# Performance work log

Measured on AMD Instinct MI355X. Metric: run time of the kernel, lower is better.

Reference implementation:

```python
import jax, jax.numpy as jnp
import numpy as np

CLS_W = 1.0
REG_W = 1.0
POS_THR = 0.6
THR_LOW = 0.3
THR_HIGH = 0.6
N_POS = 16
N_NEG = 48
BATCH = 4096
NUM_ANCHOR = 5
FS = 17
SEARCH = 255


def make_anchors():
    # SiamRPN-style anchors: 5 aspect ratios, base size 64, stride 8, 17x17 grid
    ratios = np.array([0.33, 0.5, 1.0, 2.0, 3.0], dtype=np.float64)
    size, stride = 64.0, 8
    ws = np.sqrt(size * size / ratios)            # (K,)
    hs = ws * ratios                              # (K,)
    c = (np.arange(FS) - FS // 2) * stride + SEARCH // 2  # grid centers
    cx = np.broadcast_to(c[None, None, :], (NUM_ANCHOR, FS, FS))
    cy = np.broadcast_to(c[None, :, None], (NUM_ANCHOR, FS, FS))
    w = np.broadcast_to(ws[:, None, None], (NUM_ANCHOR, FS, FS))
    h = np.broadcast_to(hs[:, None, None], (NUM_ANCHOR, FS, FS))
    center = np.stack([cx, cy, w, h], 0).reshape(4, -1).T               # (A,4) cx,cy,w,h
    corner = np.stack([cx - w / 2, cy - h / 2, cx + w / 2, cy + h / 2], 0).reshape(4, -1).T
    return center.astype(np.float32), corner.astype(np.float32)


def setup_inputs() -> dict:
    key = jax.random.key(0)
    k1, k2, k3, k4 = jax.random.split(key, 4)
    pred_cls = jax.random.normal(k1, (BATCH, NUM_ANCHOR, FS, FS), dtype=jnp.float32)
    pred_reg = jax.random.normal(k2, (BATCH, 4, NUM_ANCHOR, FS, FS), dtype=jnp.float32)
    # valid GT boxes inside the search region, overlapping anchor sizes
    cxy = jax.random.uniform(k3, (BATCH, 2), minval=90.0, maxval=165.0)
    wh = jax.random.uniform(k4, (BATCH, 2), minval=35.0, maxval=110.0)
    gt_bbox = jnp.concatenate([cxy - wh / 2, cxy + wh / 2], axis=1).astype(jnp.float32)
    center, corner = make_anchors()
    return {
        "pred_cls": pred_cls,
        "pred_reg": pred_reg,
        "gt_bbox": gt_bbox,
        "anchor_center": jnp.asarray(center),
        "anchor_corner": jnp.asarray(corner),
    }


def jaccard(box_a, box_b):
    # box_a (N,4), box_b (A,4) in x1,y1,x2,y2 -> (N,A) IoU
    lt = jnp.maximum(box_a[:, None, :2], box_b[None, :, :2])
    rb = jnp.minimum(box_a[:, None, 2:], box_b[None, :, 2:])
    wh = jnp.clip(rb - lt, 0.0)
    inter = wh[..., 0] * wh[..., 1]
    area_a = (box_a[:, 2] - box_a[:, 0]) * (box_a[:, 3] - box_a[:, 1])
    area_b = (box_b[:, 2] - box_b[:, 0]) * (box_b[:, 3] - box_b[:, 1])
    return inter / (area_a[:, None] + area_b[None, :] - inter)


def _rand_rank(k, m, A):
    # rank of each index among masked entries under a random shuffle
    u = jax.random.uniform(k, (A,))
    s = jnp.where(m, u, jnp.inf)
    order = jnp.argsort(s)
    return jnp.zeros((A,), jnp.int32).at[order].set(jnp.arange(A, dtype=jnp.int32))


def _forward(pred_cls, pred_reg, gt_bbox, anchor_center, anchor_corner):
    N = pred_cls.shape[0]
    A = anchor_center.shape[0]
    iou = jaccard(gt_bbox, anchor_corner)                       # (N,A)
    matched = jnp.where(iou > THR_HIGH, 1.0, jnp.where(iou < THR_LOW, 0.0, -1.0))
    ks = jax.random.split(jax.random.key(42), 2 * N)
    kpos, kneg = ks[:N], ks[N:]

    def per_sample(cls, reg, gt, mask, kp, kn):
        clsf = cls.reshape(-1)                                  # (A,)
        regf = reg.reshape(4, -1).T                             # (A,4)
        pos = mask == 1.0
        neg = mask == 0.0
        n_pos = jnp.sum(pos).astype(jnp.int32)
        n_neg = jnp.sum(neg).astype(jnp.int32)
        rp = _rand_rank(kp, pos, A)
        rn = _rand_rank(kn, neg, A)
        k_p = jnp.minimum(n_pos, N_POS)                         # sampled positives
        k_n_cap = jnp.where(n_pos > 0, 3 * n_pos, N_NEG)        # int(n_pos*48/16) = 3*n_pos
        k_n = jnp.minimum(n_neg, k_n_cap)
        sel_p = pos & (rp < k_p)
        sel_n = neg & (rn < k_n)
        bce_p = jnp.logaddexp(0.0, -clsf)                       # BCEWithLogits, target 1
        bce_n = jnp.logaddexp(0.0, clsf)                        # BCEWithLogits, target 0
        denom = jnp.maximum(k_p + k_n, 1).astype(clsf.dtype)
        loss_cls_i = (jnp.sum(bce_p * sel_p) + jnp.sum(bce_n * sel_n)) / denom
        acc_i = (jnp.sum((clsf >= POS_THR) & pos) + jnp.sum((clsf < POS_THR) & (~pos))).astype(clsf.dtype) / A
        gcx = (gt[0] + gt[2]) * 0.5
        gcy = (gt[1] + gt[3]) * 0.5
        gw = gt[2] - gt[0]
        gh = gt[3] - gt[1]
        acx, acy, aw, ah = anchor_center[:, 0], anchor_center[:, 1], anchor_center[:, 2], anchor_center[:, 3]
        tgt = jnp.stack([(gcx - acx) / aw, (gcy - acy) / ah, jnp.log(gw / aw), jnp.log(gh / ah)], axis=1)
        np_safe = jnp.maximum(n_pos, 1).astype(clsf.dtype)
        loss_reg_i = jnp.where(n_pos > 0,
                               jnp.sum(((regf - tgt) ** 2) * pos[:, None]) / (4.0 * np_safe),
                               0.0)
        return loss_cls_i, loss_reg_i, acc_i

    lc, lr, ac = jax.vmap(per_sample)(pred_cls, pred_reg, gt_bbox, matched, kpos, kneg)
    loss_cls = jnp.mean(lc)
    loss_reg = jnp.mean(lr)
    acc_cls = jnp.mean(ac)
    loss_total = CLS_W * loss_cls + REG_W * loss_reg
    return loss_total, loss_cls, loss_reg, acc_cls


def reference(pred_cls, pred_reg, gt_bbox, anchor_center, anchor_corner):
    return _forward(pred_cls, pred_reg, gt_bbox, anchor_center, anchor_corner)
```

## Files before the change

kernel.cpp:

```cpp
#include <hip/hip_runtime.h>
#include <stdint.h>
#include <math.h>


#define A_TOT 1445
#define NITER 23
#define WPB 4
#define POS_MAX 64
#define CAND_MAX 128

__device__ __forceinline__ void tf2x32(uint32_t k0, uint32_t k1, uint32_t x0, uint32_t x1,
                                       uint32_t& o0, uint32_t& o1)
{
  const uint32_t k2 = k0 ^ k1 ^ 0x1BD11BDAu;
  x0 += k0; x1 += k1;
#define TFR(r) { x0 += x1; x1 = __builtin_rotateleft32(x1, (r)); x1 ^= x0; }
  TFR(13) TFR(15) TFR(26) TFR(6)
  x0 += k1; x1 += k2 + 1u;
  TFR(17) TFR(29) TFR(16) TFR(24)
  x0 += k2; x1 += k0 + 2u;
  TFR(13) TFR(15) TFR(26) TFR(6)
  x0 += k0; x1 += k1 + 3u;
  TFR(17) TFR(29) TFR(16) TFR(24)
  x0 += k1; x1 += k2 + 4u;
  TFR(13) TFR(15) TFR(26) TFR(6)
  x0 += k2; x1 += k0 + 5u;
#undef TFR
  o0 = x0; o1 = x1;
}

__device__ __forceinline__ float lae0(float x){
  return fmaxf(x, 0.0f) + __logf(1.0f + __expf(-fabsf(x)));
}

__global__ void __launch_bounds__(WPB * 64, 4) rpn_loss_kernel(
    const float* __restrict__ pred_cls, const float* __restrict__ pred_reg,
    const float* __restrict__ gt_bbox, const float* __restrict__ anchor_center,
    const float* __restrict__ anchor_corner,
    float* __restrict__ part,
    int N)
{
  __shared__ uint32_t s_hist[WPB][256];
  __shared__ uint32_t s_cand[WPB][CAND_MAX];
  __shared__ uint32_t s_pidx[WPB][POS_MAX];
  __shared__ float    s_pcls[WPB][POS_MAX];
  __shared__ uint32_t s_cnt[WPB][2];

  const int w    = threadIdx.x >> 6;
  const int lane = threadIdx.x & 63;
  const int n    = blockIdx.x * WPB + w;

  #pragma unroll
  for (int b = 0; b < 4; b++) s_hist[w][lane * 4 + b] = 0u;
  if (lane < 2) s_cnt[w][lane] = 0u;

  const float g0 = gt_bbox[4 * n + 0];
  const float g1 = gt_bbox[4 * n + 1];
  const float g2 = gt_bbox[4 * n + 2];
  const float g3 = gt_bbox[4 * n + 3];
  const float area_a = (g2 - g0) * (g3 - g1);

  uint32_t kp0, kp1, kn0, kn1;
  tf2x32(0u, 42u, 0u, (uint32_t)n,       kp0, kp1);
  tf2x32(0u, 42u, 0u, (uint32_t)(N + n), kn0, kn1);

  const float*  cls_base = pred_cls + (size_t)n * A_TOT;
  const float4* cornv = (const float4*)anchor_corner;

  uint32_t rn[NITER];
  float    cv[NITER];
  uint32_t negbits = 0u;
  float accc = 0.0f;

  #pragma unroll
  for (int t = 0; t < NITER; t++){
    int j = lane + 64 * t;
    bool valid = (j < A_TOT);
    int jc = valid ? j : (A_TOT - 1);
    float4 cr = cornv[jc];
    float c = cls_base[jc];
    cv[t] = c;
    float ltx = fmaxf(g0, cr.x), lty = fmaxf(g1, cr.y);
    float rbx = fminf(g2, cr.z), rby = fminf(g3, cr.w);
    float inter = fmaxf(rbx - ltx, 0.0f) * fmaxf(rby - lty, 0.0f);
    float area_b = (cr.z - cr.x) * (cr.w - cr.y);
    float iou = inter / (area_a + area_b - inter);
    bool pos = valid && (iou > 0.6f);
    bool neg = valid && (iou < 0.3f);
    uint32_t o0, o1;
    tf2x32(kn0, kn1, 0u, (uint32_t)j, o0, o1);
    uint32_t r = (o0 ^ o1) >> 9;
    rn[t] = r;
    if (neg){ negbits |= (1u << t); atomicAdd(&s_hist[w][r >> 15], 1u); }
    if (pos){
      uint32_t id = atomicAdd(&s_cnt[w][0], 1u);
      if (id < POS_MAX){ s_pidx[w][id] = (uint32_t)j; s_pcls[w][id] = c; }
    }
    if (valid) accc += ((c >= 0.6f) == pos) ? 1.0f : 0.0f;
  }

  const int n_pos = min((int)s_cnt[w][0], POS_MAX);
  const int k_p = min(n_pos, 16);

  uint32_t S0, S1, S2, S3;
  {
    int b = lane * 4;
    uint32_t v0 = s_hist[w][b], v1 = s_hist[w][b+1], v2 = s_hist[w][b+2], v3 = s_hist[w][b+3];
    S0 = v0; S1 = S0 + v1; S2 = S1 + v2; S3 = S2 + v3;
    uint32_t x = S3;
    #pragma unroll
    for (int off = 1; off < 64; off <<= 1){
      uint32_t tmp = __shfl_up(x, off, 64);
      if (lane >= off) x += tmp;
    }
    uint32_t excl = x - S3;
    S0 += excl; S1 += excl; S2 += excl; S3 += excl;
    s_hist[w][b] = S0; s_hist[w][b+1] = S1; s_hist[w][b+2] = S2; s_hist[w][b+3] = S3;
  }
  const int n_neg = (int)__shfl(S3, 63, 64);
  const int k_n = min(n_neg, (n_pos > 0) ? 3 * n_pos : 48);

  int Bb = 256, m = 0;
  if (k_n > 0){
    unsigned long long bal = __ballot(S3 >= (uint32_t)k_n);
    int fl = __ffsll((unsigned long long)bal) - 1;
    uint32_t t0 = __shfl(S0, fl, 64), t1 = __shfl(S1, fl, 64), t2 = __shfl(S2, fl, 64);
    int sub = (t0 >= (uint32_t)k_n) ? 0 : ((t1 >= (uint32_t)k_n) ? 1 : ((t2 >= (uint32_t)k_n) ? 2 : 3));
    Bb = fl * 4 + sub;
    uint32_t before = (Bb == 0) ? 0u : s_hist[w][Bb - 1];
    m = k_n - (int)before;
  }

  float lc = 0.0f, lr = 0.0f;
  if (n_pos > 0){
    uint32_t myr = 0u, myj = 0u; float myc = 0.0f;
    if (lane < n_pos){
      myj = s_pidx[w][lane];
      myc = s_pcls[w][lane];
      uint32_t o0, o1;
      tf2x32(kp0, kp1, 0u, myj, o0, o1);
      myr = (o0 ^ o1) >> 9;
    }
    int rank = 0;
    for (int l = 0; l < n_pos; l++){
      uint32_t r2 = __shfl(myr, l, 64), j2 = __shfl(myj, l, 64);
      if (lane < n_pos && (r2 < myr || (r2 == myr && j2 < myj))) rank++;
    }
    if (lane < n_pos){
      if (rank < k_p) lc += lae0(-myc);
      float gcx = (g0 + g2) * 0.5f, gcy = (g1 + g3) * 0.5f;
      float gw = g2 - g0, gh = g3 - g1;
      float4 ce = ((const float4*)anchor_center)[myj];
      const float* reg_base = pred_reg + (size_t)n * 4 * A_TOT;
      float t0 = (gcx - ce.x) / ce.z;
      float t1 = (gcy - ce.y) / ce.w;
      float t2 = __logf(gw / ce.z);
      float t3 = __logf(gh / ce.w);
      float d0 = reg_base[myj]             - t0;
      float d1 = reg_base[A_TOT + myj]     - t1;
      float d2 = reg_base[2 * A_TOT + myj] - t2;
      float d3 = reg_base[3 * A_TOT + myj] - t3;
      lr = d0 * d0 + d1 * d1 + d2 * d2 + d3 * d3;
    }
  }

  if (k_n > 0){
    #pragma unroll
    for (int t = 0; t < NITER; t++){
      if (negbits & (1u << t)){
        int bin = (int)(rn[t] >> 15);
        if (bin < Bb) lc += lae0(cv[t]);
        else if (bin == Bb){
          uint32_t id = atomicAdd(&s_cnt[w][1], 1u);
          if (id < CAND_MAX)
            s_cand[w][id] = ((rn[t] & 0x7FFFu) << 11) | (uint32_t)(lane + 64 * t);
        }
      }
    }
    const int L = min((int)s_cnt[w][1], CAND_MAX);
    for (int c = lane; c < L; c += 64){
      uint32_t my = s_cand[w][c];
      int rank = 0;
      for (int l = 0; l < L; l++) rank += (s_cand[w][l] < my) ? 1 : 0;
      if (rank < m) lc += lae0(cls_base[my & 0x7FFu]);
    }
  }

  float v0 = lc, v1 = lr, v2 = accc;
  #pragma unroll
  for (int off = 32; off > 0; off >>= 1){
    v0 += __shfl_down(v0, off, 64);
    v1 += __shfl_down(v1, off, 64);
    v2 += __shfl_down(v2, off, 64);
  }
  if (lane == 0){
    int denom = k_p + k_n; if (denom < 1) denom = 1;
    part[n]         = v0 / (float)denom;
    part[N + n]     = (n_pos > 0) ? (v1 / (4.0f * (float)n_pos)) : 0.0f;
    part[2 * N + n] = v2 * (1.0f / (float)A_TOT);
  }
}

__global__ void __launch_bounds__(256) reduce_kernel(const float* __restrict__ part,
                                                     float* __restrict__ out, int N)
{
  const int tid = threadIdx.x;
  float lc = 0.0f, lr = 0.0f, ac = 0.0f;
  for (int i = tid; i < N; i += 256){
    lc += part[i];
    lr += part[N + i];
    ac += part[2 * N + i];
  }
  __shared__ float s[12];
  #pragma unroll
  for (int off = 32; off > 0; off >>= 1){
    lc += __shfl_down(lc, off, 64);
    lr += __shfl_down(lr, off, 64);
    ac += __shfl_down(ac, off, 64);
  }
  const int wave = tid >> 6, lane = tid & 63;
  if (lane == 0){ s[wave] = lc; s[4 + wave] = lr; s[8 + wave] = ac; }
  __syncthreads();
  if (tid == 0){
    float LC = s[0] + s[1] + s[2] + s[3];
    float LR = s[4] + s[5] + s[6] + s[7];
    float AC = s[8] + s[9] + s[10] + s[11];
    float inv = 1.0f / (float)N;
    LC *= inv; LR *= inv; AC *= inv;
    out[0] = LC + LR;
    out[1] = LC;
    out[2] = LR;
    out[3] = AC;
  }
}

extern "C" void kernel_launch(void* const* d_in, const int* in_sizes, int n_in,
                              void* d_out, int out_size, void* d_ws, size_t ws_size,
                              hipStream_t stream)
{
  const float* pred_cls = (const float*)d_in[0];
  const float* pred_reg = (const float*)d_in[1];
  const float* gt_bbox  = (const float*)d_in[2];
  const float* a_center = (const float*)d_in[3];
  const float* a_corner = (const float*)d_in[4];
  float* part = (float*)d_ws;
  float* out  = (float*)d_out;

  const int N = in_sizes[2] / 4;

  hipLaunchKernelGGL(rpn_loss_kernel, dim3(N / WPB), dim3(WPB * 64), 0, stream,
                     pred_cls, pred_reg, gt_bbox, a_center, a_corner, part, N);
  hipLaunchKernelGGL(reduce_kernel, dim3(1), dim3(256), 0, stream, part, out, N);
}
```

Before: 170.9 us.

## Split each sample across two waves and overlap positive and negative work

Each sample is now handled by two wavefronts instead of one. Each wave covers half of the anchors and writes its own histogram and positive list, and both are merged after a block barrier. One wave runs the prefix-scan and threshold search while the other computes the positive sampling and regression loss at the same time. Per-thread register arrays shrink, since cls values are reloaded instead of held, which allows a higher occupancy bound. The cost is several block-wide __syncthreads and a cross-wave reduction through shared memory.

```diff
diff --git a/kernel.cpp b/kernel.cpp
--- a/kernel.cpp
+++ b/kernel.cpp
@@ -4,9 +4,9 @@
 
 
 #define A_TOT 1445
-#define NITER 23
-#define WPB 4
-#define POS_MAX 64
+#define SPB 2
+#define NH 12
+#define POSW_MAX 32
 #define CAND_MAX 128
 
 __device__ __forceinline__ void tf2x32(uint32_t k0, uint32_t k1, uint32_t x0, uint32_t x1,
@@ -33,26 +33,31 @@
   return fmaxf(x, 0.0f) + __logf(1.0f + __expf(-fabsf(x)));
 }
 
-__global__ void __launch_bounds__(WPB * 64, 4) rpn_loss_kernel(
+__global__ void __launch_bounds__(256, 8) rpn_loss_kernel(
     const float* __restrict__ pred_cls, const float* __restrict__ pred_reg,
     const float* __restrict__ gt_bbox, const float* __restrict__ anchor_center,
     const float* __restrict__ anchor_corner,
     float* __restrict__ part,
     int N)
 {
-  __shared__ uint32_t s_hist[WPB][256];
-  __shared__ uint32_t s_cand[WPB][CAND_MAX];
-  __shared__ uint32_t s_pidx[WPB][POS_MAX];
-  __shared__ float    s_pcls[WPB][POS_MAX];
-  __shared__ uint32_t s_cnt[WPB][2];
+  __shared__ uint32_t s_hist[SPB][2][256];
+  __shared__ uint32_t s_cand[SPB][CAND_MAX];
+  __shared__ uint32_t s_pidx[SPB][2][POSW_MAX];
+  __shared__ float    s_pcls[SPB][2][POSW_MAX];
+  __shared__ uint32_t s_pcnt[SPB][2];
+  __shared__ uint32_t s_ccnt[SPB];
+  __shared__ int      s_share[SPB][3];
+  __shared__ float    s_red[SPB][2][3];
 
   const int w    = threadIdx.x >> 6;
   const int lane = threadIdx.x & 63;
-  const int n    = blockIdx.x * WPB + w;
-
-  #pragma unroll
-  for (int b = 0; b < 4; b++) s_hist[w][lane * 4 + b] = 0u;
-  if (lane < 2) s_cnt[w][lane] = 0u;
+  const int s    = w >> 1;
+  const int h    = w & 1;
+  const int n    = blockIdx.x * SPB + s;
+
+  #pragma unroll
+  for (int b = 0; b < 4; b++) s_hist[s][h][lane * 4 + b] = 0u;
+  if (lane == 0) s_pcnt[s][h] = 0u;
 
   const float g0 = gt_bbox[4 * n + 0];
   const float g1 = gt_bbox[4 * n + 1];
@@ -60,26 +65,23 @@
   const float g3 = gt_bbox[4 * n + 3];
   const float area_a = (g2 - g0) * (g3 - g1);
 
-  uint32_t kp0, kp1, kn0, kn1;
-  tf2x32(0u, 42u, 0u, (uint32_t)n,       kp0, kp1);
+  uint32_t kn0, kn1;
   tf2x32(0u, 42u, 0u, (uint32_t)(N + n), kn0, kn1);
 
   const float*  cls_base = pred_cls + (size_t)n * A_TOT;
   const float4* cornv = (const float4*)anchor_corner;
 
-  uint32_t rn[NITER];
-  float    cv[NITER];
-  uint32_t negbits = 0u;
+  uint32_t rn[NH];
   float accc = 0.0f;
-
-  #pragma unroll
-  for (int t = 0; t < NITER; t++){
-    int j = lane + 64 * t;
-    bool valid = (j < A_TOT);
-    int jc = valid ? j : (A_TOT - 1);
+  const int tbase = h * NH;
+
+  #pragma unroll
+  for (int tt = 0; tt < NH; tt++){
+    const int j = lane + 64 * (tbase + tt);
+    const bool valid = (j < A_TOT);
+    const int jc = valid ? j : (A_TOT - 1);
     float4 cr = cornv[jc];
     float c = cls_base[jc];
-    cv[t] = c;
     float ltx = fmaxf(g0, cr.x), lty = fmaxf(g1, cr.y);
     float rbx = fminf(g2, cr.z), rby = fminf(g3, cr.w);
     float inter = fmaxf(rbx - ltx, 0.0f) * fmaxf(rby - lty, 0.0f);
@@ -90,23 +92,27 @@
     uint32_t o0, o1;
     tf2x32(kn0, kn1, 0u, (uint32_t)j, o0, o1);
     uint32_t r = (o0 ^ o1) >> 9;
-    rn[t] = r;
-    if (neg){ negbits |= (1u << t); atomicAdd(&s_hist[w][r >> 15], 1u); }
+    rn[tt] = neg ? r : 0xFFFFFFFFu;
+    if (neg) atomicAdd(&s_hist[s][h][r >> 15], 1u);
     if (pos){
-      uint32_t id = atomicAdd(&s_cnt[w][0], 1u);
-      if (id < POS_MAX){ s_pidx[w][id] = (uint32_t)j; s_pcls[w][id] = c; }
+      uint32_t id = atomicAdd(&s_pcnt[s][h], 1u);
+      if (id < POSW_MAX){ s_pidx[s][h][id] = (uint32_t)j; s_pcls[s][h][id] = c; }
     }
     if (valid) accc += ((c >= 0.6f) == pos) ? 1.0f : 0.0f;
   }
-
-  const int n_pos = min((int)s_cnt[w][0], POS_MAX);
-  const int k_p = min(n_pos, 16);
-
-  uint32_t S0, S1, S2, S3;
-  {
-    int b = lane * 4;
-    uint32_t v0 = s_hist[w][b], v1 = s_hist[w][b+1], v2 = s_hist[w][b+2], v3 = s_hist[w][b+3];
-    S0 = v0; S1 = S0 + v1; S2 = S1 + v2; S3 = S2 + v3;
+  __syncthreads();
+
+  const int n_pos = min((int)s_pcnt[s][0], POSW_MAX) + min((int)s_pcnt[s][1], POSW_MAX);
+  float lc = 0.0f, lr = 0.0f;
+
+  if (h == 0){
+    if (lane == 0) s_ccnt[s] = 0u;
+    const int b = lane * 4;
+    uint32_t v0 = s_hist[s][0][b]     + s_hist[s][1][b];
+    uint32_t v1 = s_hist[s][0][b + 1] + s_hist[s][1][b + 1];
+    uint32_t v2 = s_hist[s][0][b + 2] + s_hist[s][1][b + 2];
+    uint32_t v3 = s_hist[s][0][b + 3] + s_hist[s][1][b + 3];
+    uint32_t S0 = v0, S1 = S0 + v1, S2 = S1 + v2, S3 = S2 + v3;
     uint32_t x = S3;
     #pragma unroll
     for (int off = 1; off < 64; off <<= 1){
@@ -115,73 +121,86 @@
     }
     uint32_t excl = x - S3;
     S0 += excl; S1 += excl; S2 += excl; S3 += excl;
-    s_hist[w][b] = S0; s_hist[w][b+1] = S1; s_hist[w][b+2] = S2; s_hist[w][b+3] = S3;
-  }
-  const int n_neg = (int)__shfl(S3, 63, 64);
-  const int k_n = min(n_neg, (n_pos > 0) ? 3 * n_pos : 48);
-
-  int Bb = 256, m = 0;
-  if (k_n > 0){
-    unsigned long long bal = __ballot(S3 >= (uint32_t)k_n);
-    int fl = __ffsll((unsigned long long)bal) - 1;
-    uint32_t t0 = __shfl(S0, fl, 64), t1 = __shfl(S1, fl, 64), t2 = __shfl(S2, fl, 64);
-    int sub = (t0 >= (uint32_t)k_n) ? 0 : ((t1 >= (uint32_t)k_n) ? 1 : ((t2 >= (uint32_t)k_n) ? 2 : 3));
-    Bb = fl * 4 + sub;
-    uint32_t before = (Bb == 0) ? 0u : s_hist[w][Bb - 1];
-    m = k_n - (int)before;
-  }
-
-  float lc = 0.0f, lr = 0.0f;
-  if (n_pos > 0){
-    uint32_t myr = 0u, myj = 0u; float myc = 0.0f;
-    if (lane < n_pos){
-      myj = s_pidx[w][lane];
-      myc = s_pcls[w][lane];
-      uint32_t o0, o1;
-      tf2x32(kp0, kp1, 0u, myj, o0, o1);
-      myr = (o0 ^ o1) >> 9;
-    }
-    int rank = 0;
-    for (int l = 0; l < n_pos; l++){
-      uint32_t r2 = __shfl(myr, l, 64), j2 = __shfl(myj, l, 64);
-      if (lane < n_pos && (r2 < myr || (r2 == myr && j2 < myj))) rank++;
-    }
-    if (lane < n_pos){
-      if (rank < k_p) lc += lae0(-myc);
-      float gcx = (g0 + g2) * 0.5f, gcy = (g1 + g3) * 0.5f;
-      float gw = g2 - g0, gh = g3 - g1;
-      float4 ce = ((const float4*)anchor_center)[myj];
-      const float* reg_base = pred_reg + (size_t)n * 4 * A_TOT;
-      float t0 = (gcx - ce.x) / ce.z;
-      float t1 = (gcy - ce.y) / ce.w;
-      float t2 = __logf(gw / ce.z);
-      float t3 = __logf(gh / ce.w);
-      float d0 = reg_base[myj]             - t0;
-      float d1 = reg_base[A_TOT + myj]     - t1;
-      float d2 = reg_base[2 * A_TOT + myj] - t2;
-      float d3 = reg_base[3 * A_TOT + myj] - t3;
-      lr = d0 * d0 + d1 * d1 + d2 * d2 + d3 * d3;
-    }
-  }
-
+    s_hist[s][0][b] = S0; s_hist[s][0][b+1] = S1; s_hist[s][0][b+2] = S2; s_hist[s][0][b+3] = S3;
+    const int n_neg = (int)__shfl(S3, 63, 64);
+    const int k_n_w = min(n_neg, (n_pos > 0) ? 3 * n_pos : 48);
+    int Bb_w = 256, m_w = 0;
+    if (k_n_w > 0){
+      unsigned long long bal = __ballot(S3 >= (uint32_t)k_n_w);
+      int fl = __ffsll(bal) - 1;
+      uint32_t t0 = __shfl(S0, fl, 64), t1 = __shfl(S1, fl, 64), t2 = __shfl(S2, fl, 64);
+      int sub = (t0 >= (uint32_t)k_n_w) ? 0 : ((t1 >= (uint32_t)k_n_w) ? 1 : ((t2 >= (uint32_t)k_n_w) ? 2 : 3));
+      Bb_w = fl * 4 + sub;
+      uint32_t before = (Bb_w == 0) ? 0u : s_hist[s][0][Bb_w - 1];
+      m_w = k_n_w - (int)before;
+    }
+    if (lane == 0){ s_share[s][0] = k_n_w; s_share[s][1] = Bb_w; s_share[s][2] = m_w; }
+  } else {
+    if (n_pos > 0){
+      uint32_t kp0, kp1;
+      tf2x32(0u, 42u, 0u, (uint32_t)n, kp0, kp1);
+      const int c0 = min((int)s_pcnt[s][0], POSW_MAX);
+      uint32_t myr = 0u, myj = 0u; float myc = 0.0f;
+      if (lane < n_pos){
+        const int src = (lane < c0) ? 0 : 1;
+        const int idx = (lane < c0) ? lane : (lane - c0);
+        myj = s_pidx[s][src][idx];
+        myc = s_pcls[s][src][idx];
+        uint32_t o0, o1;
+        tf2x32(kp0, kp1, 0u, myj, o0, o1);
+        myr = (o0 ^ o1) >> 9;
+      }
+      int rank = 0;
+      for (int l = 0; l < n_pos; l++){
+        uint32_t r2 = __shfl(myr, l, 64), j2 = __shfl(myj, l, 64);
+        if (lane < n_pos && (r2 < myr || (r2 == myr && j2 < myj))) rank++;
+      }
+      const int k_p = min(n_pos, 16);
+      if (lane < n_pos){
+        if (rank < k_p) lc += lae0(-myc);
+        float gcx = (g0 + g2) * 0.5f, gcy = (g1 + g3) * 0.5f;
+        float gw = g2 - g0, gh = g3 - g1;
+        float4 ce = ((const float4*)anchor_center)[myj];
+        const float* reg_base = pred_reg + (size_t)n * 4 * A_TOT;
+        float t0 = (gcx - ce.x) / ce.z;
+        float t1 = (gcy - ce.y) / ce.w;
+        float t2 = __logf(gw / ce.z);
+        float t3 = __logf(gh / ce.w);
+        float d0 = reg_base[myj]             - t0;
+        float d1 = reg_base[A_TOT + myj]     - t1;
+        float d2 = reg_base[2 * A_TOT + myj] - t2;
+        float d3 = reg_base[3 * A_TOT + myj] - t3;
+        lr = d0 * d0 + d1 * d1 + d2 * d2 + d3 * d3;
+      }
+    }
+  }
+  __syncthreads();
+
+  const int k_n = s_share[s][0];
+  const int Bb  = s_share[s][1];
   if (k_n > 0){
     #pragma unroll
-    for (int t = 0; t < NITER; t++){
-      if (negbits & (1u << t)){
-        int bin = (int)(rn[t] >> 15);
-        if (bin < Bb) lc += lae0(cv[t]);
-        else if (bin == Bb){
-          uint32_t id = atomicAdd(&s_cnt[w][1], 1u);
-          if (id < CAND_MAX)
-            s_cand[w][id] = ((rn[t] & 0x7FFFu) << 11) | (uint32_t)(lane + 64 * t);
-        }
-      }
-    }
-    const int L = min((int)s_cnt[w][1], CAND_MAX);
-    for (int c = lane; c < L; c += 64){
-      uint32_t my = s_cand[w][c];
+    for (int tt = 0; tt < NH; tt++){
+      const uint32_t r = rn[tt];
+      const int bin = (int)(r >> 15);
+      if (bin < Bb){
+        lc += lae0(cls_base[lane + 64 * (tbase + tt)]);
+      } else if (bin == Bb){
+        uint32_t id = atomicAdd(&s_ccnt[s], 1u);
+        if (id < CAND_MAX)
+          s_cand[s][id] = ((r & 0x7FFFu) << 11) | (uint32_t)(lane + 64 * (tbase + tt));
+      }
+    }
+  }
+  __syncthreads();
+
+  if (k_n > 0){
+    const int m = s_share[s][2];
+    const int L = min((int)s_ccnt[s], CAND_MAX);
+    for (int c = h * 64 + lane; c < L; c += 128){
+      uint32_t my = s_cand[s][c];
       int rank = 0;
-      for (int l = 0; l < L; l++) rank += (s_cand[w][l] < my) ? 1 : 0;
+      for (int l = 0; l < L; l++) rank += (s_cand[s][l] < my) ? 1 : 0;
       if (rank < m) lc += lae0(cls_base[my & 0x7FFu]);
     }
   }
@@ -193,11 +212,18 @@
     v1 += __shfl_down(v1, off, 64);
     v2 += __shfl_down(v2, off, 64);
   }
-  if (lane == 0){
+  if (lane == 0){ s_red[s][h][0] = v0; s_red[s][h][1] = v1; s_red[s][h][2] = v2; }
+  __syncthreads();
+
+  if (h == 0 && lane == 0){
+    float LC = s_red[s][0][0] + s_red[s][1][0];
+    float LR = s_red[s][0][1] + s_red[s][1][1];
+    float AC = s_red[s][0][2] + s_red[s][1][2];
+    const int k_p = min(n_pos, 16);
     int denom = k_p + k_n; if (denom < 1) denom = 1;
-    part[n]         = v0 / (float)denom;
-    part[N + n]     = (n_pos > 0) ? (v1 / (4.0f * (float)n_pos)) : 0.0f;
-    part[2 * N + n] = v2 * (1.0f / (float)A_TOT);
+    part[n]         = LC / (float)denom;
+    part[N + n]     = (n_pos > 0) ? (LR / (4.0f * (float)n_pos)) : 0.0f;
+    part[2 * N + n] = AC * (1.0f / (float)A_TOT);
   }
 }
 
@@ -248,7 +274,7 @@
 
   const int N = in_sizes[2] / 4;
 
-  hipLaunchKernelGGL(rpn_loss_kernel, dim3(N / WPB), dim3(WPB * 64), 0, stream,
+  hipLaunchKernelGGL(rpn_loss_kernel, dim3(N / SPB), dim3(SPB * 2 * 64), 0, stream,
                      pred_cls, pred_reg, gt_bbox, a_center, a_corner, part, N);
   hipLaunchKernelGGL(reduce_kernel, dim3(1), dim3(256), 0, stream, part, out, N);
 }
```

New measurement: 184.4 us. 1.08x slower.
